# Kernel tuning notes

Measured on AMD Instinct MI355X. Metric: run time of the kernel, lower is better.

## Reference

```python
import jax, jax.numpy as jnp
import numpy as np

B, S, D, H = 2, 2048, 1024, 16
DK = D // H


def setup_inputs() -> dict:
    key = jax.random.key(0)
    ks = jax.random.split(key, 9)
    s = 1.0 / np.sqrt(D)
    return {
        "x": jax.random.normal(ks[0], (B, S, D), dtype=jnp.float32),
        "wq": jax.random.normal(ks[1], (D, D), dtype=jnp.float32) * s,
        "bq": jax.random.normal(ks[2], (D,), dtype=jnp.float32) * 0.01,
        "wk": jax.random.normal(ks[3], (D, D), dtype=jnp.float32) * s,
        "bk": jax.random.normal(ks[4], (D,), dtype=jnp.float32) * 0.01,
        "wv": jax.random.normal(ks[5], (D, D), dtype=jnp.float32) * s,
        "bv": jax.random.normal(ks[6], (D,), dtype=jnp.float32) * 0.01,
        "wo": jax.random.normal(ks[7], (D, D), dtype=jnp.float32) * s,
        "bo": jax.random.normal(ks[8], (D,), dtype=jnp.float32) * 0.01,
    }


def reference(x, wq, bq, wk, bk, wv, bv, wo, bo):
    b, s, d = x.shape
    # Linear layers use torch convention: y = x @ W.T + b
    def proj(w, bias):
        y = jnp.einsum("bsd,ed->bse", x, w) + bias
        return y.reshape(b, s, H, DK).transpose(0, 2, 1, 3)  # (B,H,S,DK)

    q = proj(wq, bq)
    k = proj(wk, bk)
    v = proj(wv, bv)

    # Because each Q-chunk attends to the full K/V with m initialized to -inf,
    # the chunked online-softmax loop is exactly full softmax attention.
    scores = jnp.einsum("bhqd,bhkd->bhqk", q, k) / jnp.sqrt(jnp.float32(DK))
    attn = jax.nn.softmax(scores, axis=-1)
    out = jnp.einsum("bhqk,bhkd->bhqd", attn, v)  # (B,H,S,DK)

    out = out.transpose(0, 2, 1, 3).reshape(b, s, d)
    return jnp.einsum("bsd,ed->bse", out, wo) + bo
```

## Files before the change

### kernel.cpp

```cpp
#include <hip/hip_runtime.h>

typedef __attribute__((ext_vector_type(8))) short s16x8;
typedef __attribute__((ext_vector_type(4))) short s16x4;
typedef __attribute__((ext_vector_type(4))) float f32x4;

#define DEVI static __device__ __forceinline__

DEVI short f2bf(float f) {
  union { float f; unsigned u; } v; v.f = f;
  unsigned u = v.u;
  unsigned r = u + 0x7FFFu + ((u >> 16) & 1u);
  return (short)(r >> 16);
}
DEVI short f2bf_fast(float f) {
  union { float f; unsigned u; } v; v.f = f;
  return (short)((v.u + 0x8000u) >> 16);
}
DEVI float bf2f(short s) {
  union { unsigned u; float f; } v;
  v.u = ((unsigned)(unsigned short)s) << 16;
  return v.f;
}
DEVI f32x4 mfma16(s16x8 a, s16x8 b, f32x4 c) {
  return __builtin_amdgcn_mfma_f32_16x16x32_bf16(a, b, c, 0, 0, 0);
}
DEVI float fexp2(float x) {
#if __has_builtin(__builtin_amdgcn_exp2f)
  return __builtin_amdgcn_exp2f(x);
#else
  float r; asm("v_exp_f32 %0, %1" : "=v"(r) : "v"(x)); return r;
#endif
}
DEVI void gld16(const void* g, void* l) {
  __builtin_amdgcn_global_load_lds(
      (const __attribute__((address_space(1))) void*)g,
      (__attribute__((address_space(3))) void*)l, 16, 0, 0);
}

constexpr int Sc = 2048, Dc = 1024, Hc = 16, DKc = 64;
constexpr int Mc = 4096;

__global__ void detect_ker(const unsigned short* __restrict__ x, int* __restrict__ flag) {
  __shared__ int cnt;
  if (threadIdx.x == 0) cnt = 0;
  __syncthreads();
  int c = 0;
  for (int i = threadIdx.x; i < 4096; i += 256) {
    int e = (x[i] >> 7) & 0xFF;
    if (e >= 140) c++;
  }
  atomicAdd(&cnt, c);
  __syncthreads();
  if (threadIdx.x == 0) *flag = (cnt > 64) ? 1 : 0;
}

__global__ void norm_all(const void* x,
                         const void* w0, const void* w1, const void* w2, const void* w3,
                         const void* b0, const void* b1, const void* b2, const void* b3,
                         short* __restrict__ xdst, short* __restrict__ wdst,
                         float* __restrict__ bdst, const int* __restrict__ flag) {
  const int f = *flag;
  const int blk = blockIdx.x, tid = threadIdx.x;
  if (blk < 8192) {
    if (!f) return;
    const void* src; short* dst; int i;
    if (blk < 4096) {
      i = blk * 256 + tid; src = x; dst = xdst;
    } else {
      int j = (blk - 4096) * 256 + tid;
      int region = j >> 18;
      const void* ws[4] = {w0, w1, w2, w3};
      src = ws[region]; dst = wdst + (size_t)region * 1048576;
      i = j & 262143;
    }
    f32x4 v = ((const f32x4*)src)[i];
    s16x4 o;
#pragma unroll
    for (int j2 = 0; j2 < 4; ++j2) o[j2] = f2bf(v[j2]);
    ((s16x4*)dst)[i] = o;
  } else {
    const void* bs[4] = {b0, b1, b2, b3};
#pragma unroll
    for (int j = 0; j < 16; ++j) {
      int i = tid + j * 256;
      int r = i >> 10, k = i & 1023;
      bdst[i] = f ? ((const float*)bs[r])[k] : bf2f(((const short*)bs[r])[k]);
    }
  }
}

__global__ __launch_bounds__(256, 3)
void gemm_qkv(const short* __restrict__ Aorig, const short* __restrict__ Acvt,
              const short* __restrict__ W0, const short* __restrict__ W1,
              const short* __restrict__ W2, const short* __restrict__ Wcvt,
              const float* __restrict__ bias_c, short* __restrict__ outQKV,
              short* __restrict__ outV, const int* __restrict__ flag) {
  constexpr int K = Dc, N = Dc;
  const int z = blockIdx.z;
  const int f = *flag;
  const short* A = f ? Acvt : Aorig;
  const short* Wor = (z == 0) ? W0 : (z == 1) ? W1 : W2;
  const short* W = f ? (Wcvt + (size_t)z * 1048576) : Wor;
  const float* bias = bias_c + (size_t)z * N;
  const float oscale = (z == 0) ? 0.125f * 1.44269504f : 1.0f;

  __shared__ short lA[128 * 64];
  __shared__ short lB[128 * 64];

  const int tid = threadIdx.x;
  const int lane = tid & 63, wave = tid >> 6;
  const int l16 = lane & 15, quad = lane >> 4;
  const int wm0 = (wave >> 1) * 64, wn0 = (wave & 1) * 64;
  const int m0 = blockIdx.y * 128, n0 = blockIdx.x * 128;
  const int lr = lane >> 3;
  const int cg = ((lane & 7) ^ lr) * 8;
  const int x7 = l16 & 7;

  f32x4 acc[4][4] = {};

  for (int k0 = 0; k0 < K; k0 += 64) {
    __syncthreads();
#pragma unroll
    for (int it = 0; it < 4; ++it) {
      int rbase = wave * 32 + it * 8;
      gld16(&A[(size_t)(m0 + rbase + lr) * K + k0 + cg], &lA[rbase * 64]);
      gld16(&W[(size_t)(n0 + rbase + lr) * K + k0 + cg], &lB[rbase * 64]);
    }
    __syncthreads();
#pragma unroll
    for (int ks = 0; ks < 2; ++ks) {
      const int sw = ((ks * 4 + quad) ^ x7) * 8;
      s16x8 af[4], bfr[4];
#pragma unroll
      for (int i = 0; i < 4; ++i) {
        af[i]  = *(const s16x8*)&lA[(wm0 + i * 16 + l16) * 64 + sw];
        bfr[i] = *(const s16x8*)&lB[(wn0 + i * 16 + l16) * 64 + sw];
      }
#pragma unroll
      for (int mi = 0; mi < 4; ++mi)
#pragma unroll
        for (int ni = 0; ni < 4; ++ni)
          acc[mi][ni] = mfma16(af[mi], bfr[ni], acc[mi][ni]);
    }
  }

  if (z == 2) {
#pragma unroll
    for (int ni = 0; ni < 4; ++ni) {
      int n = n0 + wn0 + ni * 16 + l16;
      float bv = bias[n];
      int h = (n >> 6) & 15, dk = n & 63;
#pragma unroll
      for (int mi = 0; mi < 4; ++mi) {
        int mbase = m0 + wm0 + mi * 16 + quad * 4;
        int bb = mbase >> 11, s = mbase & 2047;
        s16x4 pk;
#pragma unroll
        for (int r = 0; r < 4; ++r) pk[r] = f2bf(acc[mi][ni][r] + bv);
        *(s16x4*)&outV[(((size_t)(bb * Hc + h)) * DKc + dk) * Sc + s] = pk;
      }
    }
    return;
  }
#pragma unroll
  for (int ni = 0; ni < 4; ++ni) {
    int n = n0 + wn0 + ni * 16 + l16;
    float bv = bias[n];
#pragma unroll
    for (int mi = 0; mi < 4; ++mi) {
#pragma unroll
      for (int r = 0; r < 4; ++r) {
        int m = m0 + wm0 + mi * 16 + quad * 4 + r;
        float v = (acc[mi][ni][r] + bv) * oscale;
        int bb = m >> 11, s = m & 2047, h = n >> 6, dk = n & 63;
        size_t idx = ((((size_t)bb * Hc + h) * Sc) + s) * DKc + dk +
                     (size_t)z * Mc * N;
        outQKV[idx] = f2bf(v);
      }
    }
  }
}

__global__ __launch_bounds__(256, 4)
void gemm_out(const short* __restrict__ A, const short* __restrict__ Worig,
              const short* __restrict__ Wcvt, const float* __restrict__ bias,
              void* __restrict__ out, const int* __restrict__ flag) {
  constexpr int K = Dc, N = Dc;
  const int f = *flag;
  const short* W = f ? Wcvt : Worig;

  __shared__ short lA[64 * 64];
  __shared__ short lB[64 * 64];

  const int tid = threadIdx.x;
  const int lane = tid & 63, wave = tid >> 6;
  const int l16 = lane & 15, quad = lane >> 4;
  const int lr = lane >> 3;
  const int cg = ((lane & 7) ^ lr) * 8;
  const int x7 = l16 & 7;
  const int wm0 = (wave >> 1) * 32, wn0 = (wave & 1) * 32;
  const int m0 = blockIdx.y * 64, n0 = blockIdx.x * 64;

  f32x4 acc[2][2] = {};

  for (int k0 = 0; k0 < K; k0 += 64) {
    __syncthreads();
#pragma unroll
    for (int it = 0; it < 2; ++it) {
      int rbase = wave * 16 + it * 8;
      gld16(&A[(size_t)(m0 + rbase + lr) * K + k0 + cg], &lA[rbase * 64]);
      gld16(&W[(size_t)(n0 + rbase + lr) * K + k0 + cg], &lB[rbase * 64]);
    }
    __syncthreads();
#pragma unroll
    for (int ks = 0; ks < 2; ++ks) {
      const int sw = ((ks * 4 + quad) ^ x7) * 8;
      s16x8 af[2], bfr[2];
#pragma unroll
      for (int i = 0; i < 2; ++i) {
        af[i]  = *(const s16x8*)&lA[(wm0 + i * 16 + l16) * 64 + sw];
        bfr[i] = *(const s16x8*)&lB[(wn0 + i * 16 + l16) * 64 + sw];
      }
#pragma unroll
      for (int mi = 0; mi < 2; ++mi)
#pragma unroll
        for (int ni = 0; ni < 2; ++ni)
          acc[mi][ni] = mfma16(af[mi], bfr[ni], acc[mi][ni]);
    }
  }

#pragma unroll
  for (int ni = 0; ni < 2; ++ni) {
    int n = n0 + wn0 + ni * 16 + l16;
    float bv = bias[n];
#pragma unroll
    for (int mi = 0; mi < 2; ++mi) {
#pragma unroll
      for (int r = 0; r < 4; ++r) {
        int m = m0 + wm0 + mi * 16 + quad * 4 + r;
        float v = acc[mi][ni][r] + bv;
        if (f) ((float*)out)[(size_t)m * N + n] = v;
        else   ((short*)out)[(size_t)m * N + n] = f2bf(v);
      }
    }
  }
}

__global__ __launch_bounds__(512, 4)
void attn_ker(const short* __restrict__ Q, const short* __restrict__ Kg,
              const short* __restrict__ Vt, short* __restrict__ O) {
  __shared__ short lK[2][64 * 64];
  __shared__ short lV[2][64 * 64];
  __shared__ short lP[8][16][72];

  const int tid = threadIdx.x;
  const int lane = tid & 63, wave = tid >> 6;
  const int l16 = lane & 15, quad = lane >> 4;
  const int lr = lane >> 3;
  const int cg = ((lane & 7) ^ lr) * 8;
  const int x7 = l16 & 7;

  const int bh = blockIdx.x;
  const short* Qb = Q + (size_t)bh * Sc * DKc;
  const short* Kb = Kg + (size_t)bh * Sc * DKc;
  const short* Vb = Vt + (size_t)bh * DKc * Sc;

  const int q0 = blockIdx.y * 128 + wave * 16;

  s16x8 qf[2];
#pragma unroll
  for (int ks = 0; ks < 2; ++ks)
    qf[ks] = *(const s16x8*)&Qb[(size_t)(q0 + l16) * DKc + ks * 32 + quad * 8];

  s16x8 ones = {};
  if (l16 == 0) {
#pragma unroll
    for (int j = 0; j < 8; ++j) ones[j] = (short)0x3F80;
  }
  const f32x4 initC = {-24.f, -24.f, -24.f, -24.f};

  f32x4 oacc[4] = {};
  f32x4 oln = {};

#define STAGE(BUF, KB)                                                          \
  {                                                                             \
    int rbase = wave * 8;                                                       \
    gld16(&Kb[(size_t)((KB) + rbase + lr) * DKc + cg], &lK[BUF][rbase * 64]);   \
    gld16(&Vb[(size_t)(rbase + lr) * Sc + (KB) + cg], &lV[BUF][rbase * 64]);    \
  }

  STAGE(0, 0)

  for (int kt = 0; kt < Sc / 64; ++kt) {
    const int p = kt & 1;
    __syncthreads();
    if (kt + 1 < Sc / 64) STAGE(p ^ 1, (kt + 1) * 64)

    f32x4 sacc[4];
    {
      const int sw0 = (quad ^ x7) * 8;
      s16x8 kf[4];
#pragma unroll
      for (int ni = 0; ni < 4; ++ni)
        kf[ni] = *(const s16x8*)&lK[p][(ni * 16 + l16) * 64 + sw0];
#pragma unroll
      for (int ni = 0; ni < 4; ++ni)
        sacc[ni] = mfma16(qf[0], kf[ni], initC);
    }
    {
      const int sw1 = ((4 + quad) ^ x7) * 8;
      s16x8 kf[4];
#pragma unroll
      for (int ni = 0; ni < 4; ++ni)
        kf[ni] = *(const s16x8*)&lK[p][(ni * 16 + l16) * 64 + sw1];
#pragma unroll
      for (int ni = 0; ni < 4; ++ni)
        sacc[ni] = mfma16(qf[1], kf[ni], sacc[ni]);
    }

#pragma unroll
    for (int r = 0; r < 4; ++r) {
      int row = quad * 4 + r;
#pragma unroll
      for (int ni = 0; ni < 4; ++ni)
        lP[wave][row][ni * 16 + l16] = f2bf_fast(fexp2(sacc[ni][r]));
    }

    s16x8 vf[2][4];
#pragma unroll
    for (int ks = 0; ks < 2; ++ks) {
      const int sw = ((ks * 4 + quad) ^ x7) * 8;
#pragma unroll
      for (int ni = 0; ni < 4; ++ni)
        vf[ks][ni] = *(const s16x8*)&lV[p][(ni * 16 + l16) * 64 + sw];
    }

    __builtin_amdgcn_s_waitcnt(0xc07f);

    s16x8 pf[2];
#pragma unroll
    for (int ks = 0; ks < 2; ++ks)
      pf[ks] = *(const s16x8*)&lP[wave][l16][ks * 32 + quad * 8];

#pragma unroll
    for (int ks = 0; ks < 2; ++ks) {
#pragma unroll
      for (int ni = 0; ni < 4; ++ni)
        oacc[ni] = mfma16(pf[ks], vf[ks][ni], oacc[ni]);
      oln = mfma16(pf[ks], ones, oln);
    }
  }
#undef STAGE

  const int bb = bh >> 4, h = bh & 15;
#pragma unroll
  for (int r = 0; r < 4; ++r) {
    float l = __shfl(oln[r], lane & 48);
    float inv = 1.0f / l;
    int srow = q0 + quad * 4 + r;
#pragma unroll
    for (int ni = 0; ni < 4; ++ni) {
      int col = h * DKc + ni * 16 + l16;
      O[((size_t)(bb * Sc + srow)) * Dc + col] = f2bf(oacc[ni][r] * inv);
    }
  }
}

extern "C" void kernel_launch(void* const* d_in, const int* in_sizes, int n_in,
                              void* d_out, int out_size, void* d_ws, size_t ws_size,
                              hipStream_t stream) {
  const void* x  = d_in[0];
  const void* wq = d_in[1]; const void* bq = d_in[2];
  const void* wk = d_in[3]; const void* bk = d_in[4];
  const void* wv = d_in[5]; const void* bv = d_in[6];
  const void* wo = d_in[7]; const void* bo = d_in[8];

  char* wsb = (char*)d_ws;
  int*   flag = (int*)wsb;
  short* x_c  = (short*)(wsb + 1024);
  short* w_c  = x_c + (size_t)4 * 1024 * 1024;
  float* b_c  = (float*)(wsb + 1024 + 16 * 1024 * 1024);
  short* Qc   = (short*)(wsb + 1024 + 16 * 1024 * 1024 + 16384);
  short* Kc   = Qc + (size_t)4 * 1024 * 1024;
  short* Vtc  = Kc + (size_t)4 * 1024 * 1024;
  short* Oc   = Vtc + (size_t)4 * 1024 * 1024;

  detect_ker<<<1, 256, 0, stream>>>((const unsigned short*)x, flag);

  norm_all<<<8193, 256, 0, stream>>>(x, wq, wk, wv, wo, bq, bk, bv, bo,
                                     x_c, w_c, b_c, flag);

  gemm_qkv<<<dim3(8, 32, 3), 256, 0, stream>>>(
      (const short*)x, x_c,
      (const short*)wq, (const short*)wk, (const short*)wv, w_c,
      b_c, Qc, Vtc, flag);

  attn_ker<<<dim3(32, 16), 512, 0, stream>>>(Qc, Kc, Vtc, Oc);

  gemm_out<<<dim3(16, 64), 256, 0, stream>>>(
      Oc, (const short*)wo, w_c + 3 * 1048576, b_c + 3 * 1024, d_out, flag);
}
```

Before: 198.7 us.

## Give each wave two query tiles in attention and enlarge output GEMM M-tile

The attention kernel now runs 4 waves per block, each handling 32 query rows (two 16-row MFMA tiles) instead of 8 waves with 16 rows. Each K/V fragment read from LDS is therefore reused across two query tiles, halving LDS fragment traffic per unit of MFMA work. The output GEMM tile grows from 64x64 to 128x64 so more MFMAs run per W load, and launch bounds are lowered to 2 blocks per CU. The cost is more registers per thread and fewer waves to hide latency, plus a grid of only 512 blocks for gemm_out.

```diff
diff --git a/kernel.cpp b/kernel.cpp
--- a/kernel.cpp
+++ b/kernel.cpp
@@ -89,7 +89,7 @@
   }
 }
 
-__global__ __launch_bounds__(256, 3)
+__global__ __launch_bounds__(256, 2)
 void gemm_qkv(const short* __restrict__ Aorig, const short* __restrict__ Acvt,
               const short* __restrict__ W0, const short* __restrict__ W1,
               const short* __restrict__ W2, const short* __restrict__ Wcvt,
@@ -181,7 +181,7 @@
   }
 }
 
-__global__ __launch_bounds__(256, 4)
+__global__ __launch_bounds__(256, 2)
 void gemm_out(const short* __restrict__ A, const short* __restrict__ Worig,
               const short* __restrict__ Wcvt, const float* __restrict__ bias,
               void* __restrict__ out, const int* __restrict__ flag) {
@@ -189,7 +189,7 @@
   const int f = *flag;
   const short* W = f ? Wcvt : Worig;
 
-  __shared__ short lA[64 * 64];
+  __shared__ short lA[128 * 64];
   __shared__ short lB[64 * 64];
 
   const int tid = threadIdx.x;
@@ -198,31 +198,36 @@
   const int lr = lane >> 3;
   const int cg = ((lane & 7) ^ lr) * 8;
   const int x7 = l16 & 7;
-  const int wm0 = (wave >> 1) * 32, wn0 = (wave & 1) * 32;
-  const int m0 = blockIdx.y * 64, n0 = blockIdx.x * 64;
-
-  f32x4 acc[2][2] = {};
+  const int wm0 = (wave >> 1) * 64, wn0 = (wave & 1) * 32;
+  const int m0 = blockIdx.y * 128, n0 = blockIdx.x * 64;
+
+  f32x4 acc[4][2] = {};
 
   for (int k0 = 0; k0 < K; k0 += 64) {
     __syncthreads();
 #pragma unroll
+    for (int it = 0; it < 4; ++it) {
+      int rbase = wave * 32 + it * 8;
+      gld16(&A[(size_t)(m0 + rbase + lr) * K + k0 + cg], &lA[rbase * 64]);
+    }
+#pragma unroll
     for (int it = 0; it < 2; ++it) {
       int rbase = wave * 16 + it * 8;
-      gld16(&A[(size_t)(m0 + rbase + lr) * K + k0 + cg], &lA[rbase * 64]);
       gld16(&W[(size_t)(n0 + rbase + lr) * K + k0 + cg], &lB[rbase * 64]);
     }
     __syncthreads();
 #pragma unroll
     for (int ks = 0; ks < 2; ++ks) {
       const int sw = ((ks * 4 + quad) ^ x7) * 8;
-      s16x8 af[2], bfr[2];
-#pragma unroll
-      for (int i = 0; i < 2; ++i) {
-        af[i]  = *(const s16x8*)&lA[(wm0 + i * 16 + l16) * 64 + sw];
+      s16x8 af[4], bfr[2];
+#pragma unroll
+      for (int i = 0; i < 4; ++i)
+        af[i] = *(const s16x8*)&lA[(wm0 + i * 16 + l16) * 64 + sw];
+#pragma unroll
+      for (int i = 0; i < 2; ++i)
         bfr[i] = *(const s16x8*)&lB[(wn0 + i * 16 + l16) * 64 + sw];
-      }
-#pragma unroll
-      for (int mi = 0; mi < 2; ++mi)
+#pragma unroll
+      for (int mi = 0; mi < 4; ++mi)
 #pragma unroll
         for (int ni = 0; ni < 2; ++ni)
           acc[mi][ni] = mfma16(af[mi], bfr[ni], acc[mi][ni]);
@@ -234,7 +239,7 @@
     int n = n0 + wn0 + ni * 16 + l16;
     float bv = bias[n];
 #pragma unroll
-    for (int mi = 0; mi < 2; ++mi) {
+    for (int mi = 0; mi < 4; ++mi) {
 #pragma unroll
       for (int r = 0; r < 4; ++r) {
         int m = m0 + wm0 + mi * 16 + quad * 4 + r;
@@ -246,12 +251,12 @@
   }
 }
 
-__global__ __launch_bounds__(512, 4)
+__global__ __launch_bounds__(256, 2)
 void attn_ker(const short* __restrict__ Q, const short* __restrict__ Kg,
               const short* __restrict__ Vt, short* __restrict__ O) {
   __shared__ short lK[2][64 * 64];
   __shared__ short lV[2][64 * 64];
-  __shared__ short lP[8][16][72];
+  __shared__ short lP[4][32][72];
 
   const int tid = threadIdx.x;
   const int lane = tid & 63, wave = tid >> 6;
@@ -265,12 +270,14 @@
   const short* Kb = Kg + (size_t)bh * Sc * DKc;
   const short* Vb = Vt + (size_t)bh * DKc * Sc;
 
-  const int q0 = blockIdx.y * 128 + wave * 16;
-
-  s16x8 qf[2];
-#pragma unroll
-  for (int ks = 0; ks < 2; ++ks)
-    qf[ks] = *(const s16x8*)&Qb[(size_t)(q0 + l16) * DKc + ks * 32 + quad * 8];
+  const int q0 = blockIdx.y * 128 + wave * 32;
+
+  s16x8 qf[2][2];
+#pragma unroll
+  for (int mi = 0; mi < 2; ++mi)
+#pragma unroll
+    for (int ks = 0; ks < 2; ++ks)
+      qf[mi][ks] = *(const s16x8*)&Qb[(size_t)(q0 + mi * 16 + l16) * DKc + ks * 32 + quad * 8];
 
   s16x8 ones = {};
   if (l16 == 0) {
@@ -279,14 +286,17 @@
   }
   const f32x4 initC = {-24.f, -24.f, -24.f, -24.f};
 
-  f32x4 oacc[4] = {};
-  f32x4 oln = {};
+  f32x4 oacc[2][4] = {};
+  f32x4 oln[2] = {};
 
 #define STAGE(BUF, KB)                                                          \
   {                                                                             \
-    int rbase = wave * 8;                                                       \
-    gld16(&Kb[(size_t)((KB) + rbase + lr) * DKc + cg], &lK[BUF][rbase * 64]);   \
-    gld16(&Vb[(size_t)(rbase + lr) * Sc + (KB) + cg], &lV[BUF][rbase * 64]);    \
+    _Pragma("unroll")                                                           \
+    for (int it = 0; it < 2; ++it) {                                            \
+      int rbase = wave * 16 + it * 8;                                           \
+      gld16(&Kb[(size_t)((KB) + rbase + lr) * DKc + cg], &lK[BUF][rbase * 64]); \
+      gld16(&Vb[(size_t)(rbase + lr) * Sc + (KB) + cg], &lV[BUF][rbase * 64]);  \
+    }                                                                           \
   }
 
   STAGE(0, 0)
@@ -296,7 +306,7 @@
     __syncthreads();
     if (kt + 1 < Sc / 64) STAGE(p ^ 1, (kt + 1) * 64)
 
-    f32x4 sacc[4];
+    f32x4 sacc[2][4];
     {
       const int sw0 = (quad ^ x7) * 8;
       s16x8 kf[4];
@@ -304,8 +314,10 @@
       for (int ni = 0; ni < 4; ++ni)
         kf[ni] = *(const s16x8*)&lK[p][(ni * 16 + l16) * 64 + sw0];
 #pragma unroll
-      for (int ni = 0; ni < 4; ++ni)
-        sacc[ni] = mfma16(qf[0], kf[ni], initC);
+      for (int mi = 0; mi < 2; ++mi)
+#pragma unroll
+        for (int ni = 0; ni < 4; ++ni)
+          sacc[mi][ni] = mfma16(qf[mi][0], kf[ni], initC);
     }
     {
       const int sw1 = ((4 + quad) ^ x7) * 8;
@@ -314,17 +326,21 @@
       for (int ni = 0; ni < 4; ++ni)
         kf[ni] = *(const s16x8*)&lK[p][(ni * 16 + l16) * 64 + sw1];
 #pragma unroll
-      for (int ni = 0; ni < 4; ++ni)
-        sacc[ni] = mfma16(qf[1], kf[ni], sacc[ni]);
-    }
-
-#pragma unroll
-    for (int r = 0; r < 4; ++r) {
-      int row = quad * 4 + r;
-#pragma unroll
-      for (int ni = 0; ni < 4; ++ni)
-        lP[wave][row][ni * 16 + l16] = f2bf_fast(fexp2(sacc[ni][r]));
-    }
+      for (int mi = 0; mi < 2; ++mi)
+#pragma unroll
+        for (int ni = 0; ni < 4; ++ni)
+          sacc[mi][ni] = mfma16(qf[mi][1], kf[ni], sacc[mi][ni]);
+    }
+
+#pragma unroll
+    for (int mi = 0; mi < 2; ++mi)
+#pragma unroll
+      for (int r = 0; r < 4; ++r) {
+        int row = mi * 16 + quad * 4 + r;
+#pragma unroll
+        for (int ni = 0; ni < 4; ++ni)
+          lP[wave][row][ni * 16 + l16] = f2bf_fast(fexp2(sacc[mi][ni][r]));
+      }
 
     s16x8 vf[2][4];
 #pragma unroll
@@ -337,31 +353,39 @@
 
     __builtin_amdgcn_s_waitcnt(0xc07f);
 
-    s16x8 pf[2];
-#pragma unroll
-    for (int ks = 0; ks < 2; ++ks)
-      pf[ks] = *(const s16x8*)&lP[wave][l16][ks * 32 + quad * 8];
+    s16x8 pf[2][2];
+#pragma unroll
+    for (int mi = 0; mi < 2; ++mi)
+#pragma unroll
+      for (int ks = 0; ks < 2; ++ks)
+        pf[mi][ks] = *(const s16x8*)&lP[wave][mi * 16 + l16][ks * 32 + quad * 8];
 
 #pragma unroll
     for (int ks = 0; ks < 2; ++ks) {
 #pragma unroll
-      for (int ni = 0; ni < 4; ++ni)
-        oacc[ni] = mfma16(pf[ks], vf[ks][ni], oacc[ni]);
-      oln = mfma16(pf[ks], ones, oln);
+      for (int mi = 0; mi < 2; ++mi) {
+#pragma unroll
+        for (int ni = 0; ni < 4; ++ni)
+          oacc[mi][ni] = mfma16(pf[mi][ks], vf[ks][ni], oacc[mi][ni]);
+        oln[mi] = mfma16(pf[mi][ks], ones, oln[mi]);
+      }
     }
   }
 #undef STAGE
 
   const int bb = bh >> 4, h = bh & 15;
 #pragma unroll
-  for (int r = 0; r < 4; ++r) {
-    float l = __shfl(oln[r], lane & 48);
-    float inv = 1.0f / l;
-    int srow = q0 + quad * 4 + r;
-#pragma unroll
-    for (int ni = 0; ni < 4; ++ni) {
-      int col = h * DKc + ni * 16 + l16;
-      O[((size_t)(bb * Sc + srow)) * Dc + col] = f2bf(oacc[ni][r] * inv);
+  for (int mi = 0; mi < 2; ++mi) {
+#pragma unroll
+    for (int r = 0; r < 4; ++r) {
+      float l = __shfl(oln[mi][r], lane & 48);
+      float inv = 1.0f / l;
+      int srow = q0 + mi * 16 + quad * 4 + r;
+#pragma unroll
+      for (int ni = 0; ni < 4; ++ni) {
+        int col = h * DKc + ni * 16 + l16;
+        O[((size_t)(bb * Sc + srow)) * Dc + col] = f2bf(oacc[mi][ni][r] * inv);
+      }
     }
   }
 }
@@ -395,8 +419,8 @@
       (const short*)wq, (const short*)wk, (const short*)wv, w_c,
       b_c, Qc, Vtc, flag);
 
-  attn_ker<<<dim3(32, 16), 512, 0, stream>>>(Qc, Kc, Vtc, Oc);
-
-  gemm_out<<<dim3(16, 64), 256, 0, stream>>>(
+  attn_ker<<<dim3(32, 16), 256, 0, stream>>>(Qc, Kc, Vtc, Oc);
+
+  gemm_out<<<dim3(16, 32), 256, 0, stream>>>(
       Oc, (const short*)wo, w_c + 3 * 1048576, b_c + 3 * 1024, d_out, flag);
 }
```

Measured after the change: 206.6 us. +4.0%, slower.

## Inline dtype detection per kernel and drop detect kernel and bias staging

Applied to the files above, without the earlier changes.

Removes the separate single-block detection kernel and the flag buffer. Each kernel now detects fp32 inputs itself with a wave ballot over the first 64 halfwords of x. Biases are read directly from the inputs in the GEMM epilogues instead of being staged through a converted buffer. The QKV GEMM grid is also transposed so consecutive blocks walk M rather than N, and its launch bounds drop from 3 to 2 waves per SIMD. This saves one launch and a serial dependency, at the cost of a redundant tiny load per block and a weaker detection heuristic that samples 64 values instead of 4096.

```diff
diff --git a/kernel.cpp b/kernel.cpp
--- a/kernel.cpp
+++ b/kernel.cpp
@@ -37,71 +37,52 @@
       (__attribute__((address_space(3))) void*)l, 16, 0, 0);
 }
 
+DEVI int is_fp32(const void* x) {
+  unsigned short h = ((const unsigned short*)x)[threadIdx.x & 63];
+  int e = (h >> 7) & 0xFF;
+  unsigned long long m = __ballot(e >= 140);
+  return __popcll(m) > 2;
+}
+
 constexpr int Sc = 2048, Dc = 1024, Hc = 16, DKc = 64;
 constexpr int Mc = 4096;
 
-__global__ void detect_ker(const unsigned short* __restrict__ x, int* __restrict__ flag) {
-  __shared__ int cnt;
-  if (threadIdx.x == 0) cnt = 0;
-  __syncthreads();
-  int c = 0;
-  for (int i = threadIdx.x; i < 4096; i += 256) {
-    int e = (x[i] >> 7) & 0xFF;
-    if (e >= 140) c++;
-  }
-  atomicAdd(&cnt, c);
-  __syncthreads();
-  if (threadIdx.x == 0) *flag = (cnt > 64) ? 1 : 0;
-}
-
 __global__ void norm_all(const void* x,
                          const void* w0, const void* w1, const void* w2, const void* w3,
-                         const void* b0, const void* b1, const void* b2, const void* b3,
-                         short* __restrict__ xdst, short* __restrict__ wdst,
-                         float* __restrict__ bdst, const int* __restrict__ flag) {
-  const int f = *flag;
+                         short* __restrict__ xdst, short* __restrict__ wdst) {
+  if (!is_fp32(x)) return;
   const int blk = blockIdx.x, tid = threadIdx.x;
-  if (blk < 8192) {
-    if (!f) return;
-    const void* src; short* dst; int i;
-    if (blk < 4096) {
-      i = blk * 256 + tid; src = x; dst = xdst;
-    } else {
-      int j = (blk - 4096) * 256 + tid;
-      int region = j >> 18;
-      const void* ws[4] = {w0, w1, w2, w3};
-      src = ws[region]; dst = wdst + (size_t)region * 1048576;
-      i = j & 262143;
-    }
-    f32x4 v = ((const f32x4*)src)[i];
-    s16x4 o;
-#pragma unroll
-    for (int j2 = 0; j2 < 4; ++j2) o[j2] = f2bf(v[j2]);
-    ((s16x4*)dst)[i] = o;
+  const void* src; short* dst; int i;
+  if (blk < 4096) {
+    i = blk * 256 + tid; src = x; dst = xdst;
   } else {
-    const void* bs[4] = {b0, b1, b2, b3};
-#pragma unroll
-    for (int j = 0; j < 16; ++j) {
-      int i = tid + j * 256;
-      int r = i >> 10, k = i & 1023;
-      bdst[i] = f ? ((const float*)bs[r])[k] : bf2f(((const short*)bs[r])[k]);
-    }
-  }
-}
-
-__global__ __launch_bounds__(256, 3)
-void gemm_qkv(const short* __restrict__ Aorig, const short* __restrict__ Acvt,
+    int j = (blk - 4096) * 256 + tid;
+    int region = j >> 18;
+    const void* ws[4] = {w0, w1, w2, w3};
+    src = ws[region]; dst = wdst + (size_t)region * 1048576;
+    i = j & 262143;
+  }
+  f32x4 v = ((const f32x4*)src)[i];
+  s16x4 o;
+#pragma unroll
+  for (int j2 = 0; j2 < 4; ++j2) o[j2] = f2bf(v[j2]);
+  ((s16x4*)dst)[i] = o;
+}
+
+__global__ __launch_bounds__(256, 2)
+void gemm_qkv(const void* __restrict__ xraw, const short* __restrict__ Acvt,
               const short* __restrict__ W0, const short* __restrict__ W1,
               const short* __restrict__ W2, const short* __restrict__ Wcvt,
-              const float* __restrict__ bias_c, short* __restrict__ outQKV,
-              short* __restrict__ outV, const int* __restrict__ flag) {
+              const void* __restrict__ B0, const void* __restrict__ B1,
+              const void* __restrict__ B2, short* __restrict__ outQKV,
+              short* __restrict__ outV) {
   constexpr int K = Dc, N = Dc;
   const int z = blockIdx.z;
-  const int f = *flag;
-  const short* A = f ? Acvt : Aorig;
+  const int f = is_fp32(xraw);
+  const short* A = f ? Acvt : (const short*)xraw;
   const short* Wor = (z == 0) ? W0 : (z == 1) ? W1 : W2;
   const short* W = f ? (Wcvt + (size_t)z * 1048576) : Wor;
-  const float* bias = bias_c + (size_t)z * N;
+  const void* Bz = (z == 0) ? B0 : (z == 1) ? B1 : B2;
   const float oscale = (z == 0) ? 0.125f * 1.44269504f : 1.0f;
 
   __shared__ short lA[128 * 64];
@@ -111,7 +92,7 @@
   const int lane = tid & 63, wave = tid >> 6;
   const int l16 = lane & 15, quad = lane >> 4;
   const int wm0 = (wave >> 1) * 64, wn0 = (wave & 1) * 64;
-  const int m0 = blockIdx.y * 128, n0 = blockIdx.x * 128;
+  const int m0 = blockIdx.x * 128, n0 = blockIdx.y * 128;
   const int lr = lane >> 3;
   const int cg = ((lane & 7) ^ lr) * 8;
   const int x7 = l16 & 7;
@@ -148,7 +129,7 @@
 #pragma unroll
     for (int ni = 0; ni < 4; ++ni) {
       int n = n0 + wn0 + ni * 16 + l16;
-      float bv = bias[n];
+      float bv = f ? ((const float*)Bz)[n] : bf2f(((const short*)Bz)[n]);
       int h = (n >> 6) & 15, dk = n & 63;
 #pragma unroll
       for (int mi = 0; mi < 4; ++mi) {
@@ -165,7 +146,7 @@
 #pragma unroll
   for (int ni = 0; ni < 4; ++ni) {
     int n = n0 + wn0 + ni * 16 + l16;
-    float bv = bias[n];
+    float bv = f ? ((const float*)Bz)[n] : bf2f(((const short*)Bz)[n]);
 #pragma unroll
     for (int mi = 0; mi < 4; ++mi) {
 #pragma unroll
@@ -182,11 +163,11 @@
 }
 
 __global__ __launch_bounds__(256, 4)
-void gemm_out(const short* __restrict__ A, const short* __restrict__ Worig,
-              const short* __restrict__ Wcvt, const float* __restrict__ bias,
-              void* __restrict__ out, const int* __restrict__ flag) {
+void gemm_out(const void* __restrict__ xraw, const short* __restrict__ A,
+              const short* __restrict__ Worig, const short* __restrict__ Wcvt,
+              const void* __restrict__ Bo, void* __restrict__ out) {
   constexpr int K = Dc, N = Dc;
-  const int f = *flag;
+  const int f = is_fp32(xraw);
   const short* W = f ? Wcvt : Worig;
 
   __shared__ short lA[64 * 64];
@@ -232,7 +213,7 @@
 #pragma unroll
   for (int ni = 0; ni < 2; ++ni) {
     int n = n0 + wn0 + ni * 16 + l16;
-    float bv = bias[n];
+    float bv = f ? ((const float*)Bo)[n] : bf2f(((const short*)Bo)[n]);
 #pragma unroll
     for (int mi = 0; mi < 2; ++mi) {
 #pragma unroll
@@ -376,27 +357,21 @@
   const void* wo = d_in[7]; const void* bo = d_in[8];
 
   char* wsb = (char*)d_ws;
-  int*   flag = (int*)wsb;
-  short* x_c  = (short*)(wsb + 1024);
+  short* x_c  = (short*)(wsb);
   short* w_c  = x_c + (size_t)4 * 1024 * 1024;
-  float* b_c  = (float*)(wsb + 1024 + 16 * 1024 * 1024);
-  short* Qc   = (short*)(wsb + 1024 + 16 * 1024 * 1024 + 16384);
+  short* Qc   = w_c + (size_t)4 * 1048576;
   short* Kc   = Qc + (size_t)4 * 1024 * 1024;
   short* Vtc  = Kc + (size_t)4 * 1024 * 1024;
   short* Oc   = Vtc + (size_t)4 * 1024 * 1024;
 
-  detect_ker<<<1, 256, 0, stream>>>((const unsigned short*)x, flag);
-
-  norm_all<<<8193, 256, 0, stream>>>(x, wq, wk, wv, wo, bq, bk, bv, bo,
-                                     x_c, w_c, b_c, flag);
-
-  gemm_qkv<<<dim3(8, 32, 3), 256, 0, stream>>>(
-      (const short*)x, x_c,
-      (const short*)wq, (const short*)wk, (const short*)wv, w_c,
-      b_c, Qc, Vtc, flag);
+  norm_all<<<8192, 256, 0, stream>>>(x, wq, wk, wv, wo, x_c, w_c);
+
+  gemm_qkv<<<dim3(32, 8, 3), 256, 0, stream>>>(
+      x, x_c, (const short*)wq, (const short*)wk, (const short*)wv, w_c,
+      bq, bk, bv, Qc, Vtc);
 
   attn_ker<<<dim3(32, 16), 512, 0, stream>>>(Qc, Kc, Vtc, Oc);
 
   gemm_out<<<dim3(16, 64), 256, 0, stream>>>(
-      Oc, (const short*)wo, w_c + 3 * 1048576, b_c + 3 * 1024, d_out, flag);
-}
+      x, Oc, (const short*)wo, w_c + 3 * 1048576, bo, d_out);
+}
```

Result: faster. 188.2 us (-5.3%).
